# Optimization experiments

Hardware: AMD Instinct MI355X
Metric: run time of the kernel (lower is better)

## Reference

```python
import jax, jax.numpy as jnp
import numpy as np

MEL = 80  # seq2seq_dim


def gru_step(x, h, Wg, bg, Wc, bc):
    """TF GRUCell: gates=[r,u], new_h = u*h + (1-u)*c."""
    gates = jax.nn.sigmoid(jnp.concatenate([x, h], axis=-1) @ Wg + bg)
    r, u = jnp.split(gates, 2, axis=-1)
    c = jnp.tanh(jnp.concatenate([x, r * h], axis=-1) @ Wc + bc)
    return u * h + (1.0 - u) * c


def setup_inputs() -> dict:
    key = jax.random.key(0)
    B, T_enc, D_enc = 128, 1024, 256
    n_styles, style_dim = 10, 256
    reduc, T_dec = 5, 250
    ks = jax.random.split(key, 20)
    rn = lambda k, shape, s=0.05: jax.random.normal(k, shape, jnp.float32) * s
    return {
        "encoder_output": rn(ks[0], (B, T_enc, D_enc), 1.0),
        "inp_mask": jax.random.randint(ks[1], (B,), 1, T_enc + 1, dtype=jnp.int32),
        "inp_att": jax.nn.softmax(rn(ks[2], (B, n_styles), 1.0), axis=-1),
        "style_token": rn(ks[3], (n_styles, style_dim)),
        # decoder prenet 80->256->128
        "pre_W1": rn(ks[4], (MEL, 256)), "pre_b1": jnp.zeros((256,), jnp.float32),
        "pre_W2": rn(ks[5], (256, 128)), "pre_b2": jnp.zeros((128,), jnp.float32),
        # attention GRU cell: input = [context(256), prenet(128)] = 384, hidden 256
        "att_Wg": rn(ks[6], (384 + 256, 512)), "att_bg": jnp.ones((512,), jnp.float32),
        "att_Wc": rn(ks[7], (384 + 256, 256)), "att_bc": jnp.zeros((256,), jnp.float32),
        # Bahdanau attention (depth 256)
        "attn_Wk": rn(ks[8], (256, 256)), "attn_bk": jnp.zeros((256,), jnp.float32),
        "attn_Wq": rn(ks[9], (256, 256)), "attn_bq": jnp.zeros((256,), jnp.float32),
        "attn_v": rn(ks[10], (256,)),
        # dec_input dense: [att_out(256), weighting_context(256)] -> 256
        "deci_W": rn(ks[11], (512, 256)), "deci_b": jnp.zeros((256,), jnp.float32),
        # two residual GRU decoder layers (hidden 256)
        "dec1_Wg": rn(ks[12], (512, 512)), "dec1_bg": jnp.ones((512,), jnp.float32),
        "dec1_Wc": rn(ks[13], (512, 256)), "dec1_bc": jnp.zeros((256,), jnp.float32),
        "dec2_Wg": rn(ks[14], (512, 512)), "dec2_bg": jnp.ones((512,), jnp.float32),
        "dec2_Wc": rn(ks[15], (512, 256)), "dec2_bc": jnp.zeros((256,), jnp.float32),
        # output projection 256 -> mel*reduc
        "out_W": rn(ks[16], (256, MEL * reduc)), "out_b": jnp.zeros((MEL * reduc,), jnp.float32),
        "decode_time_steps": T_dec,
    }


def reference(encoder_output, inp_mask, inp_att, style_token,
              pre_W1, pre_b1, pre_W2, pre_b2,
              att_Wg, att_bg, att_Wc, att_bc,
              attn_Wk, attn_bk, attn_Wq, attn_bq, attn_v,
              deci_W, deci_b,
              dec1_Wg, dec1_bg, dec1_Wc, dec1_bc,
              dec2_Wg, dec2_bg, dec2_Wc, dec2_bc,
              out_W, out_b, decode_time_steps):
    B, T_enc, D = encoder_output.shape
    reduc = out_W.shape[1] // MEL
    # precompute attention keys and mask (done once in TF AttentionModule)
    keys = encoder_output @ attn_Wk + attn_bk                       # [B, T_enc, 256]
    mask = jnp.arange(T_enc)[None, :] < inp_mask[:, None]           # [B, T_enc]
    sentence_style = inp_att @ style_token                          # [B, 256]
    abs_style = jnp.abs(sentence_style)

    carry0 = (
        jnp.zeros((B, 256), jnp.float32),   # att GRU state
        jnp.zeros((B, 256), jnp.float32),   # dec GRU layer 1 state
        jnp.zeros((B, 256), jnp.float32),   # dec GRU layer 2 state
        jnp.zeros((B, 256), jnp.float32),   # last context
        jnp.zeros((B, MEL), jnp.float32),   # go frame / last output
    )

    def step(carry, _):
        h_att, h1, h2, ctx, last_out = carry
        # decoder prenet (dropout inactive, training=False)
        p = jax.nn.relu(last_out @ pre_W1 + pre_b1)
        p = jax.nn.relu(p @ pre_W2 + pre_b2)
        # attention RNN
        h_att = gru_step(jnp.concatenate([ctx, p], axis=-1), h_att,
                         att_Wg, att_bg, att_Wc, att_bc)
        # Bahdanau attention with query = attention cell state
        q = h_att @ attn_Wq + attn_bq                               # [B, 256]
        e = jnp.einsum('btd,d->bt', jnp.tanh(keys + q[:, None, :]), attn_v)
        e = jnp.where(mask, e, -1e9)
        alpha = jax.nn.softmax(e, axis=-1)                          # [B, T_enc]
        context = jnp.einsum('bt,btd->bd', alpha, encoder_output)   # [B, 256]
        # style-weighted context
        wctx = context + sentence_style
        weight_per = jnp.mean(abs_style / (jnp.abs(context) + abs_style))
        # decoder RNN: dense then 2 residual GRU layers
        dec_in = jnp.concatenate([h_att, wctx], axis=-1) @ deci_W + deci_b
        h1 = gru_step(dec_in, h1, dec1_Wg, dec1_bg, dec1_Wc, dec1_bc)
        o1 = h1 + dec_in
        h2 = gru_step(o1, h2, dec2_Wg, dec2_bg, dec2_Wc, dec2_bc)
        o2 = h2 + o1
        dense_out = o2 @ out_W + out_b                              # [B, mel*reduc]
        new_out = dense_out[:, -MEL:]
        return (h_att, h1, h2, context, new_out), (dense_out, alpha, weight_per)

    _, (dense_outs, alphas, weight_pers) = jax.lax.scan(
        step, carry0, None, length=decode_time_steps)
    # [T_dec, B, mel*reduc] -> [B, T_dec*reduc, mel]
    seq2seq_output = jnp.transpose(dense_outs, (1, 0, 2)).reshape(
        B, decode_time_steps * reduc, MEL)
    return seq2seq_output, alphas, weight_pers
```

## Files before the change

### kernel.cpp

```cpp
#include <hip/hip_runtime.h>
#include <cstdint>
#include <cstddef>


#define TDEC   250
#define BATCH  128

#define ALPHA_OFF  ((size_t)12800000)
#define WP_OFF     ((size_t)45568000)

#define WS_WACC_B   ((size_t)0)
#define WS_WGT_B    ((size_t)4096)
#define WGT_ELEMS   1658880
#define WS_KEYS_B   (WS_WGT_B + (size_t)WGT_ELEMS * 2)
#define WS_ENC_B    (WS_KEYS_B + (size_t)33554432 * 2)

#define OFF_PRE_W1   0
#define OFF_PRE_W2   20480
#define OFF_ATT_WG   53248
#define OFF_ATT_WC   380928
#define OFF_ATTN_WQ  544768
#define OFF_DECI_W   610304
#define OFF_DEC1_WG  741376
#define OFF_DEC1_WC  1003520
#define OFF_DEC2_WG  1134592
#define OFF_DEC2_WC  1396736
#define OFF_OUT_WP   1527808

__device__ inline float bf2f(unsigned short u){
    return __uint_as_float(((unsigned int)u) << 16);
}
__device__ inline unsigned short f2bf(float f){
    unsigned int u = __float_as_uint(f);
    u = (u + 0x7fffu + ((u >> 16) & 1u)) >> 16;
    return (unsigned short)u;
}
__device__ inline float ftanh(float x){
    float e = __expf(2.f * x);
    return 1.f - 2.f * __builtin_amdgcn_rcpf(e + 1.f);
}
__device__ inline float fsig(float x){
    return __builtin_amdgcn_rcpf(1.f + __expf(-x));
}

__device__ inline float block_reduce_sum(float v, float* red, int tid){
    #pragma unroll
    for (int off = 32; off; off >>= 1) v += __shfl_xor(v, off, 64);
    __syncthreads();
    if ((tid & 63) == 0) red[tid >> 6] = v;
    __syncthreads();
    if (tid == 0){
        float s = red[0];
        #pragma unroll
        for (int i = 1; i < 16; i++) s += red[i];
        red[16] = s;
    }
    __syncthreads();
    return red[16];
}
__device__ inline float block_reduce_max(float v, float* red, int tid){
    #pragma unroll
    for (int off = 32; off; off >>= 1) v = fmaxf(v, __shfl_xor(v, off, 64));
    __syncthreads();
    if ((tid & 63) == 0) red[tid >> 6] = v;
    __syncthreads();
    if (tid == 0){
        float s = red[0];
        #pragma unroll
        for (int i = 1; i < 16; i++) s = fmaxf(s, red[i]);
        red[16] = s;
    }
    __syncthreads();
    return red[16];
}

template<int ACT, int K, int N, int NOUT, int PARTS>
__device__ inline void gemv_bf(const unsigned short* __restrict__ W,
                               const float* __restrict__ bias,
                               const float* __restrict__ x, float* __restrict__ y,
                               float* scratch, int tid)
{
    constexpr int CH   = N / 8;
    constexpr int LG   = (CH == 16) ? 4 : (CH == 32) ? 5 : 6;
    constexpr int KCNT = K / PARTS;
    static_assert(KCNT * PARTS == K, "K must divide");
    static_assert(CH * PARTS <= 1024, "too many threads");
    const int chunk = tid & (CH - 1);
    const int part  = tid >> LG;
    if (PARTS == (1024 >> LG) || part < PARTS){
        const uint4* Wp = (const uint4*)W + (size_t)(part * KCNT) * (N / 8) + chunk;
        const float* xp = x + part * KCNT;
        float a0=0.f,a1=0.f,a2=0.f,a3=0.f,a4=0.f,a5=0.f,a6=0.f,a7=0.f;
        #pragma unroll 8
        for (int k = 0; k < KCNT; k++){
            uint4 w = Wp[(size_t)k * (N / 8)];
            float xv = xp[k];
            a0 = fmaf(__uint_as_float(w.x << 16),         xv, a0);
            a1 = fmaf(__uint_as_float(w.x & 0xffff0000u), xv, a1);
            a2 = fmaf(__uint_as_float(w.y << 16),         xv, a2);
            a3 = fmaf(__uint_as_float(w.y & 0xffff0000u), xv, a3);
            a4 = fmaf(__uint_as_float(w.z << 16),         xv, a4);
            a5 = fmaf(__uint_as_float(w.z & 0xffff0000u), xv, a5);
            a6 = fmaf(__uint_as_float(w.w << 16),         xv, a6);
            a7 = fmaf(__uint_as_float(w.w & 0xffff0000u), xv, a7);
        }
        float4* s4 = (float4*)(scratch + part * N + chunk * 8);
        s4[0] = float4{a0, a1, a2, a3};
        s4[1] = float4{a4, a5, a6, a7};
    }
    __syncthreads();
    if (tid < NOUT){
        float s = bias[tid];
        #pragma unroll
        for (int p = 0; p < PARTS; p++) s += scratch[p * N + tid];
        if      (ACT == 1) s = fsig(s);
        else if (ACT == 2) s = ftanh(s);
        else if (ACT == 3) s = fmaxf(s, 0.f);
        y[tid] = s;
    }
    __syncthreads();
}

__global__ void k_cvt_flat(const float* __restrict__ src, unsigned short* __restrict__ dst, int n){
    int i = blockIdx.x * 256 + threadIdx.x;
    if (i < n) dst[i] = f2bf(src[i]);
}
__global__ void k_cvt_pad(const float* __restrict__ src, unsigned short* __restrict__ dst){
    int i = blockIdx.x * 256 + threadIdx.x;
    int k = i >> 9, n = i & 511;
    dst[i] = (n < 400) ? f2bf(src[k * 400 + n]) : (unsigned short)0;
}

__global__ __launch_bounds__(256) void k_keys(const float* __restrict__ enc,
                                              const float* __restrict__ Wk,
                                              const float* __restrict__ bk,
                                              unsigned short* __restrict__ keysT)
{
    __shared__ __align__(16) float Wt[64 * 256];
    __shared__ float At[64 * 64];
    __shared__ unsigned short tileT[256 * 68];
    const int tid = threadIdx.x;
    const size_t row0 = (size_t)blockIdx.x * 64;
    const int dq = tid & 63;
    const int rg = tid >> 6;

    float4 acc[16];
    #pragma unroll
    for (int i = 0; i < 16; i++) acc[i] = float4{0.f, 0.f, 0.f, 0.f};

    for (int k0 = 0; k0 < 256; k0 += 64){
        __syncthreads();
        #pragma unroll
        for (int i = 0; i < 64; i++)
            Wt[i * 256 + tid] = Wk[(size_t)(k0 + i) * 256 + tid];
        #pragma unroll
        for (int i = 0; i < 16; i++){
            int idx = tid + i * 256;
            int r = idx >> 6, kk = idx & 63;
            At[idx] = enc[(row0 + r) * 256 + k0 + kk];
        }
        __syncthreads();
        for (int kk = 0; kk < 64; kk++){
            float4 w = ((const float4*)Wt)[kk * 64 + dq];
            #pragma unroll
            for (int rr = 0; rr < 16; rr++){
                float a = At[(rg * 16 + rr) * 64 + kk];
                acc[rr].x += a * w.x; acc[rr].y += a * w.y;
                acc[rr].z += a * w.z; acc[rr].w += a * w.w;
            }
        }
    }
    float4 bb = ((const float4*)bk)[dq];
    __syncthreads();
    #pragma unroll
    for (int rr = 0; rr < 16; rr++){
        int t_loc = rg * 16 + rr;
        #pragma unroll
        for (int c = 0; c < 4; c++){
            float val = (&acc[rr].x)[c] + (&bb.x)[c];
            int d = dq * 4 + c;
            tileT[d * 68 + t_loc] = f2bf(val);
        }
    }
    __syncthreads();
    const int b_ = (int)(row0 >> 10);
    const int t0 = (int)(row0 & 1023);
    #pragma unroll
    for (int i = 0; i < 16; i++){
        int flat = tid + i * 256;
        int d = flat >> 4, tq = flat & 15;
        ushort4 v = *(const ushort4*)&tileT[d * 68 + tq * 4];
        *(ushort4*)&keysT[(((size_t)(b_ * 256 + d)) << 10) + t0 + tq * 4] = v;
    }
}

struct KParams {
    const int *imask; const float *inp_att; const float *style_tok;
    const float *pre_b1, *pre_b2, *att_bg, *att_bc, *attn_bq, *attn_v;
    const float *deci_b, *dec1_bg, *dec1_bc, *dec2_bg, *dec2_bc, *out_b;
    const unsigned short *wgt;
    const unsigned short *keysT;
    const unsigned short *encb;
    float *wacc; float *out;
};

__global__ __launch_bounds__(1024, 1) void k_main(KParams p)
{
    __shared__ float h_att[256], h1[256], h2[256], ctxl[256], wctxl[256];
    __shared__ float stylel[256], astylel[256];
    __shared__ float q_l[256], v_l[256];
    __shared__ float p1_l[256], p_l[128], c_l[256], dec_in[256], o1_l[256], o2_l[256];
    __shared__ float g_l[512], xa[640], xd[512], dense_l[400], last_o[80];
    __shared__ float e_l[1024];
    __shared__ __align__(16) float scratch[8192];
    __shared__ float red[32];

    const int tid = threadIdx.x;
    const int b   = blockIdx.x;
    const int mlen = p.imask[b];

    const unsigned short* W = p.wgt;

    if (tid < 256){
        h_att[tid] = 0.f; h1[tid] = 0.f; h2[tid] = 0.f; ctxl[tid] = 0.f;
        float s = 0.f;
        #pragma unroll
        for (int k = 0; k < 10; k++) s += p.inp_att[b * 10 + k] * p.style_tok[k * 256 + tid];
        stylel[tid] = s; astylel[tid] = fabsf(s);
        v_l[tid] = p.attn_v[tid];
    }
    if (tid < 80) last_o[tid] = 0.f;
    __syncthreads();

    for (int s = 0; s < TDEC; s++){
        gemv_bf<3,  80, 256, 256, 16>(W + OFF_PRE_W1, p.pre_b1, last_o, p1_l, scratch, tid);
        gemv_bf<3, 256, 128, 128, 64>(W + OFF_PRE_W2, p.pre_b2, p1_l,  p_l,  scratch, tid);

        if (tid < 640) xa[tid] = (tid < 256) ? ctxl[tid]
                               : (tid < 384) ? p_l[tid - 256]
                               : h_att[tid - 384];
        __syncthreads();
        gemv_bf<1, 640, 512, 512, 16>(W + OFF_ATT_WG, p.att_bg, xa, g_l, scratch, tid);
        if (tid < 256) xa[384 + tid] = g_l[tid] * h_att[tid];
        __syncthreads();
        gemv_bf<2, 640, 256, 256, 32>(W + OFF_ATT_WC, p.att_bc, xa, c_l, scratch, tid);
        if (tid < 256){
            float u = g_l[256 + tid];
            h_att[tid] = u * h_att[tid] + (1.f - u) * c_l[tid];
        }
        __syncthreads();
        gemv_bf<0, 256, 256, 256, 32>(W + OFF_ATTN_WQ, p.attn_bq, h_att, q_l, scratch, tid);

        {
            const int tc   = tid & 127;
            const int part = tid >> 7;
            float acc0=0.f,acc1=0.f,acc2=0.f,acc3=0.f,acc4=0.f,acc5=0.f,acc6=0.f,acc7=0.f;
            if (tc * 8 < mlen){
                const unsigned short* kp = p.keysT + (((size_t)b) << 18)
                                         + ((size_t)(part * 32) << 10) + tc * 8;
                #pragma unroll 8
                for (int dd = 0; dd < 32; dd++){
                    uint4 kv = *(const uint4*)(kp + ((size_t)dd << 10));
                    int d = part * 32 + dd;
                    float qd = q_l[d], vd = v_l[d];
                    acc0 = fmaf(ftanh(__uint_as_float(kv.x << 16)         + qd), vd, acc0);
                    acc1 = fmaf(ftanh(__uint_as_float(kv.x & 0xffff0000u) + qd), vd, acc1);
                    acc2 = fmaf(ftanh(__uint_as_float(kv.y << 16)         + qd), vd, acc2);
                    acc3 = fmaf(ftanh(__uint_as_float(kv.y & 0xffff0000u) + qd), vd, acc3);
                    acc4 = fmaf(ftanh(__uint_as_float(kv.z << 16)         + qd), vd, acc4);
                    acc5 = fmaf(ftanh(__uint_as_float(kv.z & 0xffff0000u) + qd), vd, acc5);
                    acc6 = fmaf(ftanh(__uint_as_float(kv.w << 16)         + qd), vd, acc6);
                    acc7 = fmaf(ftanh(__uint_as_float(kv.w & 0xffff0000u) + qd), vd, acc7);
                }
            }
            float4* s4 = (float4*)(scratch + part * 1024 + tc * 8);
            s4[0] = float4{acc0, acc1, acc2, acc3};
            s4[1] = float4{acc4, acc5, acc6, acc7};
        }
        __syncthreads();
        float ev = -1e30f;
        if (tid < mlen){
            float s8 = 0.f;
            #pragma unroll
            for (int pp = 0; pp < 8; pp++) s8 += scratch[pp * 1024 + tid];
            ev = s8;
        }
        float m  = block_reduce_max(ev, red, tid);
        float a  = (tid < mlen) ? __expf(ev - m) : 0.f;
        float sm = block_reduce_sum(a, red, tid);
        float alpha = a * __builtin_amdgcn_rcpf(sm);
        e_l[tid] = alpha;
        __builtin_nontemporal_store(alpha,
            &p.out[ALPHA_OFF + (size_t)s * 131072 + ((size_t)b << 10) + tid]);
        __syncthreads();

        {
            const int dc = tid & 31;
            const int tp = tid >> 5;
            float acc0=0.f,acc1=0.f,acc2=0.f,acc3=0.f,acc4=0.f,acc5=0.f,acc6=0.f,acc7=0.f;
            const unsigned short* er = p.encb + (((size_t)b) << 18) + dc * 8;
            for (int t = tp; t < mlen; t += 32){
                uint4 ev4 = *(const uint4*)(er + ((size_t)t << 8));
                float al = e_l[t];
                acc0 = fmaf(al, __uint_as_float(ev4.x << 16),         acc0);
                acc1 = fmaf(al, __uint_as_float(ev4.x & 0xffff0000u), acc1);
                acc2 = fmaf(al, __uint_as_float(ev4.y << 16),         acc2);
                acc3 = fmaf(al, __uint_as_float(ev4.y & 0xffff0000u), acc3);
                acc4 = fmaf(al, __uint_as_float(ev4.z << 16),         acc4);
                acc5 = fmaf(al, __uint_as_float(ev4.z & 0xffff0000u), acc5);
                acc6 = fmaf(al, __uint_as_float(ev4.w << 16),         acc6);
                acc7 = fmaf(al, __uint_as_float(ev4.w & 0xffff0000u), acc7);
            }
            float4* s4 = (float4*)(scratch + tp * 256 + dc * 8);
            s4[0] = float4{acc0, acc1, acc2, acc3};
            s4[1] = float4{acc4, acc5, acc6, acc7};
        }
        __syncthreads();
        float wpv = 0.f;
        if (tid < 256){
            float cs = 0.f;
            #pragma unroll
            for (int pp = 0; pp < 32; pp++) cs += scratch[pp * 256 + tid];
            ctxl[tid]  = cs;
            wctxl[tid] = cs + stylel[tid];
            wpv = astylel[tid] * __builtin_amdgcn_rcpf(fabsf(cs) + astylel[tid]);
        }
        float wsum = block_reduce_sum(wpv, red, tid);
        if (tid == 0) atomicAdd(&p.wacc[s], wsum);

        if (tid < 512) xd[tid] = (tid < 256) ? h_att[tid] : wctxl[tid - 256];
        __syncthreads();
        gemv_bf<0, 512, 256, 256, 32>(W + OFF_DECI_W, p.deci_b, xd, dec_in, scratch, tid);

        if (tid < 512) xd[tid] = (tid < 256) ? dec_in[tid] : h1[tid - 256];
        __syncthreads();
        gemv_bf<1, 512, 512, 512, 16>(W + OFF_DEC1_WG, p.dec1_bg, xd, g_l, scratch, tid);
        if (tid < 256) xd[256 + tid] = g_l[tid] * h1[tid];
        __syncthreads();
        gemv_bf<2, 512, 256, 256, 32>(W + OFF_DEC1_WC, p.dec1_bc, xd, c_l, scratch, tid);
        if (tid < 256){
            float u = g_l[256 + tid];
            float hn = u * h1[tid] + (1.f - u) * c_l[tid];
            h1[tid] = hn; o1_l[tid] = hn + dec_in[tid];
        }
        __syncthreads();

        if (tid < 512) xd[tid] = (tid < 256) ? o1_l[tid] : h2[tid - 256];
        __syncthreads();
        gemv_bf<1, 512, 512, 512, 16>(W + OFF_DEC2_WG, p.dec2_bg, xd, g_l, scratch, tid);
        if (tid < 256) xd[256 + tid] = g_l[tid] * h2[tid];
        __syncthreads();
        gemv_bf<2, 512, 256, 256, 32>(W + OFF_DEC2_WC, p.dec2_bc, xd, c_l, scratch, tid);
        if (tid < 256){
            float u = g_l[256 + tid];
            float hn = u * h2[tid] + (1.f - u) * c_l[tid];
            h2[tid] = hn; o2_l[tid] = hn + o1_l[tid];
        }
        __syncthreads();

        gemv_bf<0, 256, 512, 400, 16>(W + OFF_OUT_WP, p.out_b, o2_l, dense_l, scratch, tid);
        if (tid < 400){
            float val = dense_l[tid];
            __builtin_nontemporal_store(val,
                &p.out[(size_t)b * 100000 + (size_t)s * 400 + tid]);
            if (tid >= 320) last_o[tid - 320] = val;
        }
        __syncthreads();
    }
}

__global__ void k_final(const float* __restrict__ wacc, float* __restrict__ out)
{
    int i = threadIdx.x;
    if (i < TDEC) out[WP_OFF + i] = wacc[i] * (1.0f / 32768.0f);
}

extern "C" void kernel_launch(void* const* d_in, const int* in_sizes, int n_in,
                              void* d_out, int out_size, void* d_ws, size_t ws_size,
                              hipStream_t stream)
{
    const float* enc        = (const float*)d_in[0];
    const int*   imask      = (const int*)  d_in[1];
    const float* inp_att    = (const float*)d_in[2];
    const float* style_tok  = (const float*)d_in[3];
    const float* pre_W1     = (const float*)d_in[4];
    const float* pre_b1     = (const float*)d_in[5];
    const float* pre_W2     = (const float*)d_in[6];
    const float* pre_b2     = (const float*)d_in[7];
    const float* att_Wg     = (const float*)d_in[8];
    const float* att_bg     = (const float*)d_in[9];
    const float* att_Wc     = (const float*)d_in[10];
    const float* att_bc     = (const float*)d_in[11];
    const float* attn_Wk    = (const float*)d_in[12];
    const float* attn_bk    = (const float*)d_in[13];
    const float* attn_Wq    = (const float*)d_in[14];
    const float* attn_bq    = (const float*)d_in[15];
    const float* attn_v     = (const float*)d_in[16];
    const float* deci_W     = (const float*)d_in[17];
    const float* deci_b     = (const float*)d_in[18];
    const float* dec1_Wg    = (const float*)d_in[19];
    const float* dec1_bg    = (const float*)d_in[20];
    const float* dec1_Wc    = (const float*)d_in[21];
    const float* dec1_bc    = (const float*)d_in[22];
    const float* dec2_Wg    = (const float*)d_in[23];
    const float* dec2_bg    = (const float*)d_in[24];
    const float* dec2_Wc    = (const float*)d_in[25];
    const float* dec2_bc    = (const float*)d_in[26];
    const float* out_W      = (const float*)d_in[27];
    const float* out_b      = (const float*)d_in[28];

    float*          wacc  = (float*)((char*)d_ws + WS_WACC_B);
    unsigned short* wgt   = (unsigned short*)((char*)d_ws + WS_WGT_B);
    unsigned short* keysT = (unsigned short*)((char*)d_ws + WS_KEYS_B);
    unsigned short* encb  = (unsigned short*)((char*)d_ws + WS_ENC_B);
    float* out = (float*)d_out;

    hipMemsetAsync(d_ws, 0, 1024, stream);

    auto cvt = [&](const float* src, size_t off, int n){
        k_cvt_flat<<<(n + 255) / 256, 256, 0, stream>>>(src, wgt + off, n);
    };
    cvt(pre_W1,  OFF_PRE_W1,   80 * 256);
    cvt(pre_W2,  OFF_PRE_W2,  256 * 128);
    cvt(att_Wg,  OFF_ATT_WG,  640 * 512);
    cvt(att_Wc,  OFF_ATT_WC,  640 * 256);
    cvt(attn_Wq, OFF_ATTN_WQ, 256 * 256);
    cvt(deci_W,  OFF_DECI_W,  512 * 256);
    cvt(dec1_Wg, OFF_DEC1_WG, 512 * 512);
    cvt(dec1_Wc, OFF_DEC1_WC, 512 * 256);
    cvt(dec2_Wg, OFF_DEC2_WG, 512 * 512);
    cvt(dec2_Wc, OFF_DEC2_WC, 512 * 256);
    k_cvt_pad<<<(256 * 512) / 256, 256, 0, stream>>>(out_W, wgt + OFF_OUT_WP);

    k_cvt_flat<<<(33554432 + 255) / 256, 256, 0, stream>>>(enc, encb, 33554432);

    k_keys<<<2048, 256, 0, stream>>>(enc, attn_Wk, attn_bk, keysT);

    KParams kp{imask, inp_att, style_tok,
               pre_b1, pre_b2, att_bg, att_bc, attn_bq, attn_v,
               deci_b, dec1_bg, dec1_bc, dec2_bg, dec2_bc, out_b,
               wgt, keysT, encb, wacc, out};
    k_main<<<BATCH, 1024, 0, stream>>>(kp);

    k_final<<<1, 256, 0, stream>>>(wacc, out);
}
```

Before: 24.38 ms.

## Split GRU candidate matmul so input part overlaps gate matmul, trim barriers

Splits each GRU candidate GEMV into an input part that does not depend on the reset gate and a hidden part that does. The input part now runs alongside the gate GEMV in a second scratch buffer, which shortens the serial chain of barrier-separated phases. It also writes operands straight into the concatenated input buffers instead of copying them, and drops the softmax max-subtraction so one block reduction and its barriers go away. It raises some unroll factors. Skipping the max-subtraction risks exp overflow for large scores, and the extra scratch buffer increases LDS use.

```diff
diff --git a/kernel.cpp b/kernel.cpp
--- a/kernel.cpp
+++ b/kernel.cpp
@@ -19,12 +19,15 @@
 #define OFF_PRE_W2   20480
 #define OFF_ATT_WG   53248
 #define OFF_ATT_WC   380928
+#define OFF_ATT_WCH  479232
 #define OFF_ATTN_WQ  544768
 #define OFF_DECI_W   610304
 #define OFF_DEC1_WG  741376
 #define OFF_DEC1_WC  1003520
+#define OFF_DEC1_WCH 1069056
 #define OFF_DEC2_WG  1134592
 #define OFF_DEC2_WC  1396736
+#define OFF_DEC2_WCH 1462272
 #define OFF_OUT_WP   1527808
 
 __device__ inline float bf2f(unsigned short u){
@@ -43,42 +46,10 @@
     return __builtin_amdgcn_rcpf(1.f + __expf(-x));
 }
 
-__device__ inline float block_reduce_sum(float v, float* red, int tid){
-    #pragma unroll
-    for (int off = 32; off; off >>= 1) v += __shfl_xor(v, off, 64);
-    __syncthreads();
-    if ((tid & 63) == 0) red[tid >> 6] = v;
-    __syncthreads();
-    if (tid == 0){
-        float s = red[0];
-        #pragma unroll
-        for (int i = 1; i < 16; i++) s += red[i];
-        red[16] = s;
-    }
-    __syncthreads();
-    return red[16];
-}
-__device__ inline float block_reduce_max(float v, float* red, int tid){
-    #pragma unroll
-    for (int off = 32; off; off >>= 1) v = fmaxf(v, __shfl_xor(v, off, 64));
-    __syncthreads();
-    if ((tid & 63) == 0) red[tid >> 6] = v;
-    __syncthreads();
-    if (tid == 0){
-        float s = red[0];
-        #pragma unroll
-        for (int i = 1; i < 16; i++) s = fmaxf(s, red[i]);
-        red[16] = s;
-    }
-    __syncthreads();
-    return red[16];
-}
-
-template<int ACT, int K, int N, int NOUT, int PARTS>
-__device__ inline void gemv_bf(const unsigned short* __restrict__ W,
-                               const float* __restrict__ bias,
-                               const float* __restrict__ x, float* __restrict__ y,
-                               float* scratch, int tid)
+template<int K, int N, int PARTS>
+__device__ inline void gemv_part(const unsigned short* __restrict__ W,
+                                 const float* __restrict__ x,
+                                 float* __restrict__ scratch, int tid)
 {
     constexpr int CH   = N / 8;
     constexpr int LG   = (CH == 16) ? 4 : (CH == 32) ? 5 : 6;
@@ -108,17 +79,14 @@
         s4[0] = float4{a0, a1, a2, a3};
         s4[1] = float4{a4, a5, a6, a7};
     }
-    __syncthreads();
-    if (tid < NOUT){
-        float s = bias[tid];
-        #pragma unroll
-        for (int p = 0; p < PARTS; p++) s += scratch[p * N + tid];
-        if      (ACT == 1) s = fsig(s);
-        else if (ACT == 2) s = ftanh(s);
-        else if (ACT == 3) s = fmaxf(s, 0.f);
-        y[tid] = s;
-    }
-    __syncthreads();
+}
+
+template<int N, int PARTS>
+__device__ inline float red_parts(const float* __restrict__ scratch, int n){
+    float s = 0.f;
+    #pragma unroll
+    for (int p = 0; p < PARTS; p++) s += scratch[p * N + n];
+    return s;
 }
 
 __global__ void k_cvt_flat(const float* __restrict__ src, unsigned short* __restrict__ dst, int n){
@@ -206,50 +174,80 @@
 
 __global__ __launch_bounds__(1024, 1) void k_main(KParams p)
 {
-    __shared__ float h_att[256], h1[256], h2[256], ctxl[256], wctxl[256];
-    __shared__ float stylel[256], astylel[256];
-    __shared__ float q_l[256], v_l[256];
-    __shared__ float p1_l[256], p_l[128], c_l[256], dec_in[256], o1_l[256], o2_l[256];
-    __shared__ float g_l[512], xa[640], xd[512], dense_l[400], last_o[80];
+    __shared__ __align__(16) float scr [8192];
+    __shared__ __align__(16) float scr2[8192];
+    __shared__ float xa[640];
+    __shared__ float xg[512];
+    __shared__ float xr[256];
+    __shared__ float xd[512];
+    __shared__ float g_l[512], cx_l[256];
+    __shared__ float h_att[256], h1[256], h2[256];
+    __shared__ float p1_l[256], dci[256], o1_l[256], o2_l[256];
+    __shared__ float stylel[256], astylel[256], v_l[256], q_l[256];
     __shared__ float e_l[1024];
-    __shared__ __align__(16) float scratch[8192];
-    __shared__ float red[32];
+    __shared__ float last_o[80];
+    __shared__ float red[16];
 
     const int tid = threadIdx.x;
     const int b   = blockIdx.x;
     const int mlen = p.imask[b];
-
     const unsigned short* W = p.wgt;
 
     if (tid < 256){
-        h_att[tid] = 0.f; h1[tid] = 0.f; h2[tid] = 0.f; ctxl[tid] = 0.f;
+        h_att[tid] = 0.f; h1[tid] = 0.f; h2[tid] = 0.f;
         float s = 0.f;
         #pragma unroll
         for (int k = 0; k < 10; k++) s += p.inp_att[b * 10 + k] * p.style_tok[k * 256 + tid];
         stylel[tid] = s; astylel[tid] = fabsf(s);
         v_l[tid] = p.attn_v[tid];
+        xa[tid] = 0.f;
+        xa[384 + tid] = 0.f;
     }
     if (tid < 80) last_o[tid] = 0.f;
     __syncthreads();
 
     for (int s = 0; s < TDEC; s++){
-        gemv_bf<3,  80, 256, 256, 16>(W + OFF_PRE_W1, p.pre_b1, last_o, p1_l, scratch, tid);
-        gemv_bf<3, 256, 128, 128, 64>(W + OFF_PRE_W2, p.pre_b2, p1_l,  p_l,  scratch, tid);
-
-        if (tid < 640) xa[tid] = (tid < 256) ? ctxl[tid]
-                               : (tid < 384) ? p_l[tid - 256]
-                               : h_att[tid - 384];
-        __syncthreads();
-        gemv_bf<1, 640, 512, 512, 16>(W + OFF_ATT_WG, p.att_bg, xa, g_l, scratch, tid);
-        if (tid < 256) xa[384 + tid] = g_l[tid] * h_att[tid];
-        __syncthreads();
-        gemv_bf<2, 640, 256, 256, 32>(W + OFF_ATT_WC, p.att_bc, xa, c_l, scratch, tid);
+        gemv_part<80, 256, 16>(W + OFF_PRE_W1, last_o, scr, tid);
+        __syncthreads();
+        if (tid < 256)
+            p1_l[tid] = fmaxf(p.pre_b1[tid] + red_parts<256,16>(scr, tid), 0.f);
+        __syncthreads();
+
+        gemv_part<256, 128, 64>(W + OFF_PRE_W2, p1_l, scr, tid);
+        __syncthreads();
+        if (tid < 128)
+            xa[256 + tid] = fmaxf(p.pre_b2[tid] + red_parts<128,64>(scr, tid), 0.f);
+        __syncthreads();
+
+        gemv_part<640, 512, 16>(W + OFF_ATT_WG, xa, scr,  tid);
+        gemv_part<384, 256, 32>(W + OFF_ATT_WC, xa, scr2, tid);
+        __syncthreads();
+        if (tid < 512){
+            float g = fsig(p.att_bg[tid] + red_parts<512,16>(scr, tid));
+            g_l[tid] = g;
+            if (tid < 256) xr[tid] = g * h_att[tid];
+        } else if (tid < 768){
+            int n = tid - 512;
+            cx_l[n] = p.att_bc[n] + red_parts<256,32>(scr2, n);
+        }
+        __syncthreads();
+
+        gemv_part<256, 256, 32>(W + OFF_ATT_WCH, xr, scr, tid);
+        __syncthreads();
         if (tid < 256){
+            float c = ftanh(cx_l[tid] + red_parts<256,32>(scr, tid));
             float u = g_l[256 + tid];
-            h_att[tid] = u * h_att[tid] + (1.f - u) * c_l[tid];
-        }
-        __syncthreads();
-        gemv_bf<0, 256, 256, 256, 32>(W + OFF_ATTN_WQ, p.attn_bq, h_att, q_l, scratch, tid);
+            float h = u * h_att[tid] + (1.f - u) * c;
+            h_att[tid] = h;
+            xa[384 + tid] = h;
+            xd[tid] = h;
+        }
+        __syncthreads();
+
+        gemv_part<256, 256, 32>(W + OFF_ATTN_WQ, h_att, scr, tid);
+        __syncthreads();
+        if (tid < 256) q_l[tid] = p.attn_bq[tid] + red_parts<256,32>(scr, tid);
+        __syncthreads();
 
         {
             const int tc   = tid & 127;
@@ -258,7 +256,7 @@
             if (tc * 8 < mlen){
                 const unsigned short* kp = p.keysT + (((size_t)b) << 18)
                                          + ((size_t)(part * 32) << 10) + tc * 8;
-                #pragma unroll 8
+                #pragma unroll 16
                 for (int dd = 0; dd < 32; dd++){
                     uint4 kv = *(const uint4*)(kp + ((size_t)dd << 10));
                     int d = part * 32 + dd;
@@ -273,25 +271,34 @@
                     acc7 = fmaf(ftanh(__uint_as_float(kv.w & 0xffff0000u) + qd), vd, acc7);
                 }
             }
-            float4* s4 = (float4*)(scratch + part * 1024 + tc * 8);
+            float4* s4 = (float4*)(scr + part * 1024 + tc * 8);
             s4[0] = float4{acc0, acc1, acc2, acc3};
             s4[1] = float4{acc4, acc5, acc6, acc7};
         }
         __syncthreads();
-        float ev = -1e30f;
+        float av = 0.f;
         if (tid < mlen){
             float s8 = 0.f;
             #pragma unroll
-            for (int pp = 0; pp < 8; pp++) s8 += scratch[pp * 1024 + tid];
-            ev = s8;
-        }
-        float m  = block_reduce_max(ev, red, tid);
-        float a  = (tid < mlen) ? __expf(ev - m) : 0.f;
-        float sm = block_reduce_sum(a, red, tid);
-        float alpha = a * __builtin_amdgcn_rcpf(sm);
-        e_l[tid] = alpha;
-        __builtin_nontemporal_store(alpha,
-            &p.out[ALPHA_OFF + (size_t)s * 131072 + ((size_t)b << 10) + tid]);
+            for (int pp = 0; pp < 8; pp++) s8 += scr[pp * 1024 + tid];
+            av = __expf(s8);
+        }
+        {
+            float ws = av;
+            #pragma unroll
+            for (int off = 32; off; off >>= 1) ws += __shfl_xor(ws, off, 64);
+            if ((tid & 63) == 0) red[tid >> 6] = ws;
+        }
+        __syncthreads();
+        {
+            float tot = 0.f;
+            #pragma unroll
+            for (int i = 0; i < 16; i++) tot += red[i];
+            float alpha = av * __builtin_amdgcn_rcpf(tot);
+            e_l[tid] = alpha;
+            __builtin_nontemporal_store(alpha,
+                &p.out[ALPHA_OFF + (size_t)s * 131072 + ((size_t)b << 10) + tid]);
+        }
         __syncthreads();
 
         {
@@ -299,6 +306,7 @@
             const int tp = tid >> 5;
             float acc0=0.f,acc1=0.f,acc2=0.f,acc3=0.f,acc4=0.f,acc5=0.f,acc6=0.f,acc7=0.f;
             const unsigned short* er = p.encb + (((size_t)b) << 18) + dc * 8;
+            #pragma unroll 8
             for (int t = tp; t < mlen; t += 32){
                 uint4 ev4 = *(const uint4*)(er + ((size_t)t << 8));
                 float al = e_l[t];
@@ -311,56 +319,85 @@
                 acc6 = fmaf(al, __uint_as_float(ev4.w << 16),         acc6);
                 acc7 = fmaf(al, __uint_as_float(ev4.w & 0xffff0000u), acc7);
             }
-            float4* s4 = (float4*)(scratch + tp * 256 + dc * 8);
+            float4* s4 = (float4*)(scr + tp * 256 + dc * 8);
             s4[0] = float4{acc0, acc1, acc2, acc3};
             s4[1] = float4{acc4, acc5, acc6, acc7};
         }
         __syncthreads();
-        float wpv = 0.f;
         if (tid < 256){
-            float cs = 0.f;
+            float cs = red_parts<256,32>(scr, tid);
+            xa[tid] = cs;
+            xd[256 + tid] = cs + stylel[tid];
+            float wpv = astylel[tid] * __builtin_amdgcn_rcpf(fabsf(cs) + astylel[tid]);
             #pragma unroll
-            for (int pp = 0; pp < 32; pp++) cs += scratch[pp * 256 + tid];
-            ctxl[tid]  = cs;
-            wctxl[tid] = cs + stylel[tid];
-            wpv = astylel[tid] * __builtin_amdgcn_rcpf(fabsf(cs) + astylel[tid]);
-        }
-        float wsum = block_reduce_sum(wpv, red, tid);
-        if (tid == 0) atomicAdd(&p.wacc[s], wsum);
-
-        if (tid < 512) xd[tid] = (tid < 256) ? h_att[tid] : wctxl[tid - 256];
-        __syncthreads();
-        gemv_bf<0, 512, 256, 256, 32>(W + OFF_DECI_W, p.deci_b, xd, dec_in, scratch, tid);
-
-        if (tid < 512) xd[tid] = (tid < 256) ? dec_in[tid] : h1[tid - 256];
-        __syncthreads();
-        gemv_bf<1, 512, 512, 512, 16>(W + OFF_DEC1_WG, p.dec1_bg, xd, g_l, scratch, tid);
-        if (tid < 256) xd[256 + tid] = g_l[tid] * h1[tid];
-        __syncthreads();
-        gemv_bf<2, 512, 256, 256, 32>(W + OFF_DEC1_WC, p.dec1_bc, xd, c_l, scratch, tid);
+            for (int off = 32; off; off >>= 1) wpv += __shfl_xor(wpv, off, 64);
+            if ((tid & 63) == 0) atomicAdd(&p.wacc[s], wpv);
+        }
+        __syncthreads();
+
+        gemv_part<512, 256, 32>(W + OFF_DECI_W, xd, scr, tid);
+        __syncthreads();
         if (tid < 256){
+            float d = p.deci_b[tid] + red_parts<256,32>(scr, tid);
+            dci[tid] = d;
+            xg[tid] = d; xg[256 + tid] = h1[tid];
+        }
+        __syncthreads();
+
+        gemv_part<512, 512, 16>(W + OFF_DEC1_WG, xg, scr,  tid);
+        gemv_part<256, 256, 32>(W + OFF_DEC1_WC, xg, scr2, tid);
+        __syncthreads();
+        if (tid < 512){
+            float g = fsig(p.dec1_bg[tid] + red_parts<512,16>(scr, tid));
+            g_l[tid] = g;
+            if (tid < 256) xr[tid] = g * h1[tid];
+        } else if (tid < 768){
+            int n = tid - 512;
+            cx_l[n] = p.dec1_bc[n] + red_parts<256,32>(scr2, n);
+        }
+        __syncthreads();
+
+        gemv_part<256, 256, 32>(W + OFF_DEC1_WCH, xr, scr, tid);
+        __syncthreads();
+        if (tid < 256){
+            float c = ftanh(cx_l[tid] + red_parts<256,32>(scr, tid));
             float u = g_l[256 + tid];
-            float hn = u * h1[tid] + (1.f - u) * c_l[tid];
-            h1[tid] = hn; o1_l[tid] = hn + dec_in[tid];
-        }
-        __syncthreads();
-
-        if (tid < 512) xd[tid] = (tid < 256) ? o1_l[tid] : h2[tid - 256];
-        __syncthreads();
-        gemv_bf<1, 512, 512, 512, 16>(W + OFF_DEC2_WG, p.dec2_bg, xd, g_l, scratch, tid);
-        if (tid < 256) xd[256 + tid] = g_l[tid] * h2[tid];
-        __syncthreads();
-        gemv_bf<2, 512, 256, 256, 32>(W + OFF_DEC2_WC, p.dec2_bc, xd, c_l, scratch, tid);
+            float hn = u * h1[tid] + (1.f - u) * c;
+            h1[tid] = hn;
+            float o1 = hn + dci[tid];
+            o1_l[tid] = o1;
+            xg[tid] = o1; xg[256 + tid] = h2[tid];
+        }
+        __syncthreads();
+
+        gemv_part<512, 512, 16>(W + OFF_DEC2_WG, xg, scr,  tid);
+        gemv_part<256, 256, 32>(W + OFF_DEC2_WC, xg, scr2, tid);
+        __syncthreads();
+        if (tid < 512){
+            float g = fsig(p.dec2_bg[tid] + red_parts<512,16>(scr, tid));
+            g_l[tid] = g;
+            if (tid < 256) xr[tid] = g * h2[tid];
+        } else if (tid < 768){
+            int n = tid - 512;
+            cx_l[n] = p.dec2_bc[n] + red_parts<256,32>(scr2, n);
+        }
+        __syncthreads();
+
+        gemv_part<256, 256, 32>(W + OFF_DEC2_WCH, xr, scr, tid);
+        __syncthreads();
         if (tid < 256){
+            float c = ftanh(cx_l[tid] + red_parts<256,32>(scr, tid));
             float u = g_l[256 + tid];
-            float hn = u * h2[tid] + (1.f - u) * c_l[tid];
-            h2[tid] = hn; o2_l[tid] = hn + o1_l[tid];
-        }
-        __syncthreads();
-
-        gemv_bf<0, 256, 512, 400, 16>(W + OFF_OUT_WP, p.out_b, o2_l, dense_l, scratch, tid);
+            float hn = u * h2[tid] + (1.f - u) * c;
+            h2[tid] = hn;
+            o2_l[tid] = hn + o1_l[tid];
+        }
+        __syncthreads();
+
+        gemv_part<256, 512, 16>(W + OFF_OUT_WP, o2_l, scr, tid);
+        __syncthreads();
         if (tid < 400){
-            float val = dense_l[tid];
+            float val = p.out_b[tid] + red_parts<512,16>(scr, tid);
             __builtin_nontemporal_store(val,
                 &p.out[(size_t)b * 100000 + (size_t)s * 400 + tid]);
             if (tid >= 320) last_o[tid - 320] = val;
```

Result: faster. 23.70 ms (-2.8%).
